# Kernel tuning notes

Hardware: AMD Instinct MI355X
Metric: run time of the kernel (lower is better)

## Reference

```python
import jax, jax.numpy as jnp
import numpy as np

B, S, H = 2, 2048, 1024
NH, KVH, HD = 16, 4, 64
EPS = 1e-6


def setup_inputs() -> dict:
    key = jax.random.key(0)
    ks = jax.random.split(key, 6)
    hidden_states = jax.random.normal(ks[0], (B, S, H), jnp.float32)
    # additive causal mask [B,1,S,S]
    neg = jnp.finfo(jnp.float32).min
    causal = jnp.where(jnp.tril(jnp.ones((S, S), bool)), 0.0, neg)
    attention_mask = jnp.broadcast_to(causal[None, None], (B, 1, S, S))
    # RoPE cos/sin [B,S,HD]
    pos = jnp.arange(S, dtype=jnp.float32)
    inv_freq = 1.0 / (10000.0 ** (jnp.arange(0, HD, 2, dtype=jnp.float32) / HD))
    freqs = pos[:, None] * inv_freq[None, :]          # [S, HD//2]
    emb = jnp.concatenate([freqs, freqs], axis=-1)    # [S, HD]
    cos = jnp.broadcast_to(jnp.cos(emb)[None], (B, S, HD))
    sin = jnp.broadcast_to(jnp.sin(emb)[None], (B, S, HD))
    scale = 0.02
    q_weight = jax.random.normal(ks[1], (NH * HD, H), jnp.float32) * scale
    k_weight = jax.random.normal(ks[2], (KVH * HD, H), jnp.float32) * scale
    v_weight = jax.random.normal(ks[3], (KVH * HD, H), jnp.float32) * scale
    o_weight = jax.random.normal(ks[4], (H, NH * HD), jnp.float32) * scale
    q_norm_weight = jnp.ones((HD,), jnp.float32)
    k_norm_weight = jnp.ones((HD,), jnp.float32)
    return dict(hidden_states=hidden_states, attention_mask=attention_mask,
                cos=cos, sin=sin, q_weight=q_weight, k_weight=k_weight,
                v_weight=v_weight, o_weight=o_weight,
                q_norm_weight=q_norm_weight, k_norm_weight=k_norm_weight)


def _rotate_half(x):
    x1, x2 = x[..., : x.shape[-1] // 2], x[..., x.shape[-1] // 2:]
    return jnp.concatenate([-x2, x1], axis=-1)


def _rms_norm(x, w, eps=EPS):
    xf = x.astype(jnp.float32)
    var = jnp.mean(xf * xf, axis=-1, keepdims=True)
    return (w * (xf * jax.lax.rsqrt(var + eps)).astype(x.dtype))


def reference(hidden_states, attention_mask, cos, sin, q_weight, k_weight,
              v_weight, o_weight, q_norm_weight, k_norm_weight):
    b, s, h = hidden_states.shape
    # projections (torch F.linear: x @ W.T)
    q = (hidden_states @ q_weight.T).reshape(b, s, NH, HD).transpose(0, 2, 1, 3)
    k = (hidden_states @ k_weight.T).reshape(b, s, KVH, HD).transpose(0, 2, 1, 3)
    v = (hidden_states @ v_weight.T).reshape(b, s, KVH, HD).transpose(0, 2, 1, 3)
    # per-head QK RMSNorm (Qwen3 style)
    q = _rms_norm(q, q_norm_weight)
    k = _rms_norm(k, k_norm_weight)
    # RoPE, cos/sin broadcast over head axis
    c, si = cos[:, None], sin[:, None]                 # [B,1,S,HD]
    q = q * c + _rotate_half(q) * si
    k = k * c + _rotate_half(k) * si
    # GQA: repeat kv heads
    rep = NH // KVH
    k = jnp.repeat(k, rep, axis=1)
    v = jnp.repeat(v, rep, axis=1)
    # attention
    scores = jnp.einsum('bhqd,bhkd->bhqk', q, k) * (HD ** -0.5)
    scores = scores + attention_mask[:, :, :, :s]
    attn = jax.nn.softmax(scores.astype(jnp.float32), axis=-1).astype(q.dtype)
    out = jnp.einsum('bhqk,bhkd->bhqd', attn, v)
    out = out.transpose(0, 2, 1, 3).reshape(b, s, NH * HD)
    return out @ o_weight.T
```

## Files before the change

kernel.cpp:

```cpp
#include <hip/hip_runtime.h>

typedef unsigned short u16;
typedef __attribute__((ext_vector_type(4))) float f32x4;
typedef __attribute__((ext_vector_type(8))) __bf16 bf16x8;
typedef __attribute__((ext_vector_type(8))) unsigned short u16x8;
typedef __attribute__((ext_vector_type(4))) unsigned short u16x4;

#define NEGINF -3.0e38f

#define BB 2
#define SS 2048
#define HH 1024
#define NHEAD 16
#define KVHEAD 4
#define HD 64
#define BS (BB*SS)
#define NQKV 1536

#define QSCALE 0.18033688f
#define SMBIAS -11.5415603f

#define PSLOT 8320

__device__ __forceinline__ u16 f2bf(float f) {
  union { float f; unsigned int u; } v; v.f = f;
  unsigned int r = v.u + 0x7FFFu + ((v.u >> 16) & 1u);
  return (u16)(r >> 16);
}
__device__ __forceinline__ float bf2f(u16 h) {
  union { unsigned int u; float f; } v; v.u = ((unsigned int)h) << 16;
  return v.f;
}

typedef const unsigned int __attribute__((address_space(1)))* gp_t;
typedef unsigned int __attribute__((address_space(3)))* lp_t;
__device__ __forceinline__ void gload_lds16(const void* g, void* l) {
  __builtin_amdgcn_global_load_lds((gp_t)g, (lp_t)l, 16, 0, 0);
}

__global__ __launch_bounds__(256) void cvt_all(
    const float* __restrict__ h, const float* __restrict__ qw,
    const float* __restrict__ kw, const float* __restrict__ vw,
    const float* __restrict__ ow,
    u16* __restrict__ Xb, u16* __restrict__ Wqkv, u16* __restrict__ Wo) {
  long i = ((long)blockIdx.x * 256 + threadIdx.x) * 4;
  const float* src; u16* dst;
  if (i < 4194304L)      { src = h  + i;             dst = Xb   + i; }
  else if (i < 5242880L) { src = qw + (i - 4194304); dst = Wqkv + (i - 4194304); }
  else if (i < 5505024L) { src = kw + (i - 5242880); dst = Wqkv + (i - 4194304); }
  else if (i < 5767168L) { src = vw + (i - 5505024); dst = Wqkv + (i - 4194304); }
  else                   { src = ow + (i - 5767168); dst = Wo   + (i - 5767168); }
  float4 v = *(const float4*)src;
  u16x4 o;
  o.x = f2bf(v.x); o.y = f2bf(v.y); o.z = f2bf(v.z); o.w = f2bf(v.w);
  *(u16x4*)dst = o;
}

template<int EPI, int TM>
__global__ __launch_bounds__(256) void gemm_bt(
    const u16* __restrict__ A, const u16* __restrict__ Bw,
    float* __restrict__ Cf,
    u16* __restrict__ Qb, u16* __restrict__ Kb, u16* __restrict__ Vb,
    const float* __restrict__ cosb, const float* __restrict__ sinb,
    const float* __restrict__ qnw, const float* __restrict__ knw,
    int M, int N, int K)
{
  const int AM = TM / 32;
  __shared__ u16 As[2][TM * 64];
  __shared__ u16 Bs[2][128 * 64];
  const int tid = threadIdx.x;
  const int w = tid >> 6, l = tid & 63;
  const int lg = l >> 4, lc = l & 15;
  const int m0 = blockIdx.y * TM, n0 = blockIdx.x * 128;
  const int wr = (w >> 1) * (TM / 2), wc = (w & 1) * 64;

  const f32x4 vzero = {0.f, 0.f, 0.f, 0.f};
  f32x4 acc[AM][4];
#pragma unroll
  for (int i = 0; i < AM; ++i)
#pragma unroll
    for (int j = 0; j < 4; ++j) acc[i][j] = vzero;

  const u16* Ap = A + (size_t)m0 * K;
  const u16* Bp = Bw + (size_t)n0 * K;
  const int nk = K >> 6;

  const int arow = tid >> 3, ach = tid & 7;

#define GSTAGE(bufi, kt)                                                         \
  {                                                                              \
    _Pragma("unroll") for (int c = 0; c < AM; ++c) {                             \
      int row = c * 32 + arow;                                                   \
      gload_lds16(Ap + (size_t)row * K + (kt) * 64 + (ach ^ (row & 7)) * 8,      \
                  (char*)As[bufi] + c * 4096 + w * 1024);                        \
    }                                                                            \
    _Pragma("unroll") for (int c = 0; c < 4; ++c) {                              \
      int row = c * 32 + arow;                                                   \
      gload_lds16(Bp + (size_t)row * K + (kt) * 64 + (ach ^ (row & 7)) * 8,      \
                  (char*)Bs[bufi] + c * 4096 + w * 1024);                        \
    }                                                                            \
  }

  GSTAGE(0, 0)
  __syncthreads();

  for (int kt = 0; kt < nk; ++kt) {
    const int cur = kt & 1;
    if (kt + 1 < nk) GSTAGE(cur ^ 1, kt + 1)

    bf16x8 af[AM][2], bfr[4][2];
#pragma unroll
    for (int i = 0; i < AM; ++i) {
      int row = wr + i * 16 + lc;
#pragma unroll
      for (int c = 0; c < 2; ++c)
        af[i][c] = *(const bf16x8*)&As[cur][row * 64 + (((c * 4 + lg) ^ (lc & 7)) << 3)];
    }
#pragma unroll
    for (int i = 0; i < 4; ++i) {
      int row = wc + i * 16 + lc;
#pragma unroll
      for (int c = 0; c < 2; ++c)
        bfr[i][c] = *(const bf16x8*)&Bs[cur][row * 64 + (((c * 4 + lg) ^ (lc & 7)) << 3)];
    }
    __builtin_amdgcn_s_setprio(1);
#pragma unroll
    for (int c = 0; c < 2; ++c)
#pragma unroll
      for (int am = 0; am < AM; ++am)
#pragma unroll
        for (int bn = 0; bn < 4; ++bn)
          acc[am][bn] = __builtin_amdgcn_mfma_f32_16x16x32_bf16(af[am][c], bfr[bn][c], acc[am][bn], 0, 0, 0);
    __builtin_amdgcn_s_setprio(0);

    if (kt + 1 < nk) __syncthreads();
  }
#undef GSTAGE

  if (EPI == 1) {
#pragma unroll
    for (int am = 0; am < AM; ++am)
#pragma unroll
      for (int bn = 0; bn < 4; ++bn)
#pragma unroll
        for (int r = 0; r < 4; ++r) {
          int m = m0 + wr + am * 16 + lg * 4 + r;
          int n = n0 + wc + bn * 16 + lc;
          Cf[(size_t)m * N + n] = acc[am][bn][r];
        }
  } else {
    const int nb = n0 + wc;
    if (nb < 1280) {
      const bool isQ = (nb < 1024);
      const int head = isQ ? (nb >> 6) : ((nb - 1024) >> 6);
      u16* dst = isQ ? (Qb + ((size_t)head * SS) * HD)
                     : (Kb + ((size_t)head * SS) * HD);
      const size_t hstride = (size_t)(isQ ? NHEAD : KVHEAD) * SS * HD;
      const float* wt = isQ ? qnw : knw;
      const float posc = isQ ? QSCALE : 1.0f;
      float wt4[4];
#pragma unroll
      for (int bn = 0; bn < 4; ++bn) wt4[bn] = wt[bn * 16 + lc];
#pragma unroll
      for (int am = 0; am < AM; ++am)
#pragma unroll
        for (int r = 0; r < 4; ++r) {
          int m = m0 + wr + am * 16 + lg * 4 + r;
          int bb = m >> 11, s2 = m & 2047;
          float ss = 0.f;
#pragma unroll
          for (int bn = 0; bn < 4; ++bn) ss += acc[am][bn][r] * acc[am][bn][r];
          ss += __shfl_xor(ss, 1);
          ss += __shfl_xor(ss, 2);
          ss += __shfl_xor(ss, 4);
          ss += __shfl_xor(ss, 8);
          float rs = rsqrtf(ss * (1.0f / 64.0f) + 1e-6f);
          size_t cbase = ((size_t)bb * SS + s2) * HD;
          size_t obase = bb * hstride + (size_t)s2 * HD;
#pragma unroll
          for (int bn = 0; bn < 4; ++bn) {
            int d = bn * 16 + lc;
            float xn = acc[am][bn][r] * rs * wt4[bn];
            float xp = acc[am][bn ^ 2][r] * rs * wt4[bn ^ 2];
            float rot = (bn < 2) ? -xp : xp;
            float o = (xn * cosb[cbase + d] + rot * sinb[cbase + d]) * posc;
            dst[obase + d] = f2bf(o);
          }
        }
    } else {
      const int kh = (nb - 1280) >> 6;
#pragma unroll
      for (int am = 0; am < AM; ++am)
#pragma unroll
        for (int r = 0; r < 4; ++r) {
          int m = m0 + wr + am * 16 + lg * 4 + r;
          int bb = m >> 11, s2 = m & 2047;
#pragma unroll
          for (int bn = 0; bn < 4; ++bn) {
            int d = bn * 16 + lc;
            Vb[(((size_t)bb * KVHEAD + kh) * HD + d) * SS + s2] = f2bf(acc[am][bn][r]);
          }
        }
    }
  }
}

__global__ __launch_bounds__(256) void attn_kernel(
    const u16* __restrict__ Qb, const u16* __restrict__ Kb,
    const u16* __restrict__ Vt, u16* __restrict__ Ob,
    float* __restrict__ Pw)
{
  __shared__ u16 Ks[2][64 * 64];
  __shared__ u16 Vs[2][64 * 64];

  const int tid = threadIdx.x;
  const int w = tid >> 6, l = tid & 63;
  const int lg = l >> 4, lc = l & 15;

  const int bid = blockIdx.x;
  const int p = bid & 255, half = bid >> 8;
  const int qt_s = p & 7, hb = p >> 3;
  const int h = hb & 15, b = hb >> 4;
  const int qt_l = 15 - qt_s;
  const int L1 = 2 * qt_s + 2;
  const int kvh = h >> 2;

  const u16* Kp = Kb + ((size_t)b * KVHEAD + kvh) * SS * HD;
  const u16* Vp = Vt + ((size_t)b * KVHEAD + kvh) * (size_t)HD * SS;

  const f32x4 vzero = {0.f, 0.f, 0.f, 0.f};
  const f32x4 zbias = {SMBIAS, SMBIAS, SMBIAS, SMBIAS};
  f32x4 acc[2][4];
  float lsum[2] = {0.f, 0.f};
#pragma unroll
  for (int qf = 0; qf < 2; ++qf)
#pragma unroll
    for (int df = 0; df < 4; ++df) acc[qf][df] = vzero;

  const int srow0 = w * 8 + (l >> 3);
  const int srow1 = srow0 + 32;
  const int sswz = (l >> 3) ^ ((w & 1) << 2);
  const int ss0 = (l & 7) ^ sswz;

  int ko[8], vo[8];
#pragma unroll
  for (int f = 0; f < 4; ++f) {
    int row = ((lc >> 2) << 3) + ((f & 1) << 2) + (lc & 3) + ((f >> 1) << 5);
    int swz = (((f & 1) << 2) + (lc & 3)) ^ (((lc >> 2) & 1) << 2);
    ko[2 * f]     = row * 64 + ((lg ^ swz) << 3);
    ko[2 * f + 1] = row * 64 + (((4 + lg) ^ swz) << 3);
  }
#pragma unroll
  for (int df = 0; df < 4; ++df) {
    int vrow = 16 * df + lc;
    int vswz = (lc & 7) ^ (((lc >> 3) & 1) << 2);
    vo[2 * df]     = vrow * 64 + ((lg ^ vswz) << 3);
    vo[2 * df + 1] = vrow * 64 + (((4 + lg) ^ vswz) << 3);
  }

#define STAGE(bufi, kvbase)                                                          \
  gload_lds16(Kp + (size_t)((kvbase) + srow0) * HD + ss0 * 8, (char*)Ks[bufi] + w * 1024);        \
  gload_lds16(Kp + (size_t)((kvbase) + srow1) * HD + ss0 * 8, (char*)Ks[bufi] + 4096 + w * 1024); \
  gload_lds16(Vp + (size_t)srow0 * SS + (kvbase) + ss0 * 8, (char*)Vs[bufi] + w * 1024);          \
  gload_lds16(Vp + (size_t)srow1 * SS + (kvbase) + ss0 * 8, (char*)Vs[bufi] + 4096 + w * 1024);

  auto seg = [&](int qt, int lo, int hi, bool fin) {
    const int q0 = qt * 128;
    const u16* Qp = Qb + (((size_t)b * NHEAD + h) * SS + q0 + w * 32) * HD;
    bf16x8 qa[2][2];
#pragma unroll
    for (int qf = 0; qf < 2; ++qf)
#pragma unroll
      for (int c = 0; c < 2; ++c)
        qa[qf][c] = *(const bf16x8*)(Qp + (qf * 16 + lc) * HD + c * 32 + lg * 8);

    STAGE(0, lo * 64)
    __syncthreads();

    for (int t = lo; t < hi; ++t) {
      const int cur = (t - lo) & 1;
      if (t + 1 < hi) { STAGE(cur ^ 1, (t + 1) * 64) }

      const int kv0 = t * 64;
      if (kv0 <= q0 + w * 32 + 31) {
        const u16* KsB = Ks[cur];
        const u16* VsB = Vs[cur];

        bf16x8 kb[8], vb[8];
#pragma unroll
        for (int i = 0; i < 8; ++i) kb[i] = *(const bf16x8*)&KsB[ko[i]];
#pragma unroll
        for (int i = 0; i < 8; ++i) vb[i] = *(const bf16x8*)&VsB[vo[i]];

        const bool diag = (kv0 + 63 > q0 + w * 32);
        bf16x8 pa[2][2];
#pragma unroll
        for (int c = 0; c < 2; ++c) {
          f32x4 sv[2][2];
#pragma unroll
          for (int fs = 0; fs < 2; ++fs) {
            const int f = 2 * c + fs;
#pragma unroll
            for (int qf = 0; qf < 2; ++qf) {
              f32x4 z = zbias;
              z = __builtin_amdgcn_mfma_f32_16x16x32_bf16(kb[2 * f], qa[qf][0], z, 0, 0, 0);
              z = __builtin_amdgcn_mfma_f32_16x16x32_bf16(kb[2 * f + 1], qa[qf][1], z, 0, 0, 0);
              sv[qf][fs] = z;
            }
          }
          if (diag) {
            const int keyb = kv0 + c * 32 + lg * 8;
#pragma unroll
            for (int qf = 0; qf < 2; ++qf) {
              const int qi = q0 + w * 32 + qf * 16 + lc;
#pragma unroll
              for (int fs = 0; fs < 2; ++fs)
#pragma unroll
                for (int rr = 0; rr < 4; ++rr) {
                  int key = keyb + fs * 4 + rr;
                  if (key > qi) sv[qf][fs][rr] = NEGINF;
                }
            }
          }
#pragma unroll
          for (int qf = 0; qf < 2; ++qf) {
#pragma unroll
            for (int fs = 0; fs < 2; ++fs)
#pragma unroll
              for (int rr = 0; rr < 4; ++rr) {
                float pp = __builtin_amdgcn_exp2f(sv[qf][fs][rr]);
                sv[qf][fs][rr] = pp;
                lsum[qf] += pp;
              }
#pragma unroll
            for (int j = 0; j < 8; ++j)
              pa[qf][c][j] = (__bf16)sv[qf][j >> 2][j & 3];
          }
        }

#pragma unroll
        for (int df = 0; df < 4; ++df)
#pragma unroll
          for (int qf = 0; qf < 2; ++qf) {
            acc[qf][df] = __builtin_amdgcn_mfma_f32_16x16x32_bf16(pa[qf][0], vb[2 * df], acc[qf][df], 0, 0, 0);
            acc[qf][df] = __builtin_amdgcn_mfma_f32_16x16x32_bf16(pa[qf][1], vb[2 * df + 1], acc[qf][df], 0, 0, 0);
          }
      }

      __syncthreads();
    }

    if (fin) {
#pragma unroll
      for (int qf = 0; qf < 2; ++qf) {
        float t = lsum[qf];
        t += __shfl_xor(t, 16);
        t += __shfl_xor(t, 32);
#pragma unroll
        for (int rr = 0; rr < 4; ++rr) {
          float dnm = __shfl(t, lg * 4 + rr);
          float inv = 1.0f / dnm;
          int qi = q0 + w * 32 + qf * 16 + lg * 4 + rr;
#pragma unroll
          for (int df = 0; df < 4; ++df)
            Ob[((size_t)b * SS + qi) * (NHEAD * HD) + h * HD + df * 16 + lc] =
                f2bf(acc[qf][df][rr] * inv);
        }
        lsum[qf] = 0.f;
#pragma unroll
        for (int df = 0; df < 4; ++df) acc[qf][df] = vzero;
      }
    }
  };

  if (half == 0) {
    seg(qt_s, 0, L1, true);
    seg(qt_l, 0, 17 - L1, false);
  } else {
    seg(qt_l, 17 - L1, 2 * qt_l + 2, false);
  }
#undef STAGE

  float* slot = Pw + (size_t)(p * 2 + half) * PSLOT;
#pragma unroll
  for (int qf = 0; qf < 2; ++qf) {
#pragma unroll
    for (int rr = 0; rr < 4; ++rr) {
      int row = w * 32 + qf * 16 + lg * 4 + rr;
#pragma unroll
      for (int df = 0; df < 4; ++df)
        slot[row * 64 + df * 16 + lc] = acc[qf][df][rr];
    }
    float t = lsum[qf];
    t += __shfl_xor(t, 16);
    t += __shfl_xor(t, 32);
    if (l < 16) slot[8192 + w * 32 + qf * 16 + l] = t;
  }
}

__global__ __launch_bounds__(256) void attn_combine(
    const float* __restrict__ Pw, u16* __restrict__ Ob)
{
  const int blk = blockIdx.x;
  const int p = blk >> 1, rh = blk & 1;
  const int qt_s = p & 7, hb = p >> 3;
  const int h = hb & 15, b = hb >> 4;
  const int qt_l = 15 - qt_s;
  const float* A = Pw + (size_t)(p * 2 + 0) * PSLOT;
  const float* Bp = Pw + (size_t)(p * 2 + 1) * PSLOT;
#pragma unroll
  for (int i = 0; i < 16; ++i) {
    int e = i * 256 + threadIdx.x;
    int row = rh * 64 + (e >> 6), d = e & 63;
    float s = A[row * 64 + d] + Bp[row * 64 + d];
    float dn = A[8192 + row] + Bp[8192 + row];
    int qrow = qt_l * 128 + row;
    Ob[((size_t)b * SS + qrow) * (NHEAD * HD) + h * HD + d] = f2bf(s / dn);
  }
}

extern "C" void kernel_launch(void* const* d_in, const int* in_sizes, int n_in,
                              void* d_out, int out_size, void* d_ws, size_t ws_size,
                              hipStream_t stream) {
  const float* hidden = (const float*)d_in[0];
  const float* cosb = (const float*)d_in[2];
  const float* sinb = (const float*)d_in[3];
  const float* qw = (const float*)d_in[4];
  const float* kw = (const float*)d_in[5];
  const float* vw = (const float*)d_in[6];
  const float* ow = (const float*)d_in[7];
  const float* qnw = (const float*)d_in[8];
  const float* knw = (const float*)d_in[9];
  float* out = (float*)d_out;

  u16* Xb   = (u16*)d_ws;
  u16* Wqkv = Xb + (size_t)BS * HH;
  u16* Wo   = Wqkv + (size_t)NQKV * HH;
  u16* Qb   = Wo + (size_t)HH * HH;
  u16* Kb   = Qb + (size_t)BB * NHEAD * SS * HD;
  u16* Vb   = Kb + (size_t)BB * KVHEAD * SS * HD;
  u16* Ab   = Vb + (size_t)BB * KVHEAD * SS * HD;
  float* Pw = (float*)(Ab + (size_t)BS * HH);

  cvt_all<<<6656, 256, 0, stream>>>(hidden, qw, kw, vw, ow, Xb, Wqkv, Wo);

  gemm_bt<0, 128><<<dim3(NQKV / 128, BS / 128), 256, 0, stream>>>(
      Xb, Wqkv, nullptr, Qb, Kb, Vb, cosb, sinb, qnw, knw, BS, NQKV, HH);

  attn_kernel<<<512, 256, 0, stream>>>(Qb, Kb, Vb, Ab, Pw);
  attn_combine<<<512, 256, 0, stream>>>(Pw, Ab);

  gemm_bt<1, 64><<<dim3(HH / 128, BS / 64), 256, 0, stream>>>(
      Ab, Wo, out, nullptr, nullptr, nullptr, nullptr, nullptr, nullptr, nullptr, BS, HH, HH);
}
```

Before: 89.58 us.

## Split causal attention work into three balanced chunks per pair and shrink QKV GEMM tile

Attention work for each (short, long) query-tile pair is now divided across three blocks of about eleven KV tiles each, instead of two uneven halves. Every partial result goes to a workspace slot, and the combine kernel sums one to three slots per query tile. This is meant to balance load and raise occupancy on the many-CU GPU, at the cost of more partial writes and combine reads. Separately, the QKV projection GEMM switches to 64-row M tiles, which doubles its grid size.

```diff
diff --git a/kernel.cpp b/kernel.cpp
--- a/kernel.cpp
+++ b/kernel.cpp
@@ -207,8 +207,7 @@
 
 __global__ __launch_bounds__(256) void attn_kernel(
     const u16* __restrict__ Qb, const u16* __restrict__ Kb,
-    const u16* __restrict__ Vt, u16* __restrict__ Ob,
-    float* __restrict__ Pw)
+    const u16* __restrict__ Vt, float* __restrict__ Pw)
 {
   __shared__ u16 Ks[2][64 * 64];
   __shared__ u16 Vs[2][64 * 64];
@@ -218,7 +217,7 @@
   const int lg = l >> 4, lc = l & 15;
 
   const int bid = blockIdx.x;
-  const int p = bid & 255, half = bid >> 8;
+  const int p = bid & 255, ch = bid >> 8;
   const int qt_s = p & 7, hb = p >> 3;
   const int h = hb & 15, b = hb >> 4;
   const int qt_l = 15 - qt_s;
@@ -264,7 +263,7 @@
   gload_lds16(Vp + (size_t)srow0 * SS + (kvbase) + ss0 * 8, (char*)Vs[bufi] + w * 1024);          \
   gload_lds16(Vp + (size_t)srow1 * SS + (kvbase) + ss0 * 8, (char*)Vs[bufi] + 4096 + w * 1024);
 
-  auto seg = [&](int qt, int lo, int hi, bool fin) {
+  auto seg = [&](int qt, int klo, int khi) {
     const int q0 = qt * 128;
     const u16* Qp = Qb + (((size_t)b * NHEAD + h) * SS + q0 + w * 32) * HD;
     bf16x8 qa[2][2];
@@ -274,12 +273,12 @@
       for (int c = 0; c < 2; ++c)
         qa[qf][c] = *(const bf16x8*)(Qp + (qf * 16 + lc) * HD + c * 32 + lg * 8);
 
-    STAGE(0, lo * 64)
+    STAGE(0, klo * 64)
     __syncthreads();
 
-    for (int t = lo; t < hi; ++t) {
-      const int cur = (t - lo) & 1;
-      if (t + 1 < hi) { STAGE(cur ^ 1, (t + 1) * 64) }
+    for (int t = klo; t < khi; ++t) {
+      const int cur = (t - klo) & 1;
+      if (t + 1 < khi) { STAGE(cur ^ 1, (t + 1) * 64) }
 
       const int kv0 = t * 64;
       if (kv0 <= q0 + w * 32 + 31) {
@@ -349,72 +348,71 @@
 
       __syncthreads();
     }
-
-    if (fin) {
-#pragma unroll
-      for (int qf = 0; qf < 2; ++qf) {
-        float t = lsum[qf];
-        t += __shfl_xor(t, 16);
-        t += __shfl_xor(t, 32);
-#pragma unroll
-        for (int rr = 0; rr < 4; ++rr) {
-          float dnm = __shfl(t, lg * 4 + rr);
-          float inv = 1.0f / dnm;
-          int qi = q0 + w * 32 + qf * 16 + lg * 4 + rr;
-#pragma unroll
-          for (int df = 0; df < 4; ++df)
-            Ob[((size_t)b * SS + qi) * (NHEAD * HD) + h * HD + df * 16 + lc] =
-                f2bf(acc[qf][df][rr] * inv);
-        }
-        lsum[qf] = 0.f;
-#pragma unroll
-        for (int df = 0; df < 4; ++df) acc[qf][df] = vzero;
+  };
+
+  auto wslot = [&](int sidx) {
+    float* slot = Pw + (size_t)(p * 4 + sidx) * PSLOT;
+#pragma unroll
+    for (int qf = 0; qf < 2; ++qf) {
+#pragma unroll
+      for (int rr = 0; rr < 4; ++rr) {
+        int row = w * 32 + qf * 16 + lg * 4 + rr;
+#pragma unroll
+        for (int df = 0; df < 4; ++df)
+          slot[row * 64 + df * 16 + lc] = acc[qf][df][rr];
       }
+      float t = lsum[qf];
+      t += __shfl_xor(t, 16);
+      t += __shfl_xor(t, 32);
+      if (l < 16) slot[8192 + w * 32 + qf * 16 + l] = t;
+      lsum[qf] = 0.f;
+#pragma unroll
+      for (int df = 0; df < 4; ++df) acc[qf][df] = vzero;
     }
   };
 
-  if (half == 0) {
-    seg(qt_s, 0, L1, true);
-    seg(qt_l, 0, 17 - L1, false);
+  if (ch == 0) {
+    seg(qt_s, 0, (L1 < 11) ? L1 : 11);
+    wslot(0);
+    if (L1 < 11) { seg(qt_l, 0, 11 - L1); wslot(1); }
+  } else if (ch == 1) {
+    if (L1 > 11) { seg(qt_s, 11, L1); wslot(1); }
+    seg(qt_l, (L1 < 11) ? (11 - L1) : 0, 22 - L1);
+    wslot(2);
   } else {
-    seg(qt_l, 17 - L1, 2 * qt_l + 2, false);
+    seg(qt_l, 22 - L1, 34 - L1);
+    wslot(3);
   }
 #undef STAGE
-
-  float* slot = Pw + (size_t)(p * 2 + half) * PSLOT;
-#pragma unroll
-  for (int qf = 0; qf < 2; ++qf) {
-#pragma unroll
-    for (int rr = 0; rr < 4; ++rr) {
-      int row = w * 32 + qf * 16 + lg * 4 + rr;
-#pragma unroll
-      for (int df = 0; df < 4; ++df)
-        slot[row * 64 + df * 16 + lc] = acc[qf][df][rr];
-    }
-    float t = lsum[qf];
-    t += __shfl_xor(t, 16);
-    t += __shfl_xor(t, 32);
-    if (l < 16) slot[8192 + w * 32 + qf * 16 + l] = t;
-  }
 }
 
 __global__ __launch_bounds__(256) void attn_combine(
     const float* __restrict__ Pw, u16* __restrict__ Ob)
 {
   const int blk = blockIdx.x;
-  const int p = blk >> 1, rh = blk & 1;
+  const int p = blk >> 1, which = blk & 1;
   const int qt_s = p & 7, hb = p >> 3;
   const int h = hb & 15, b = hb >> 4;
-  const int qt_l = 15 - qt_s;
-  const float* A = Pw + (size_t)(p * 2 + 0) * PSLOT;
-  const float* Bp = Pw + (size_t)(p * 2 + 1) * PSLOT;
-#pragma unroll
-  for (int i = 0; i < 16; ++i) {
+  const int qt = which ? (15 - qt_s) : qt_s;
+  const float* base = Pw + (size_t)p * 4 * PSLOT;
+  const float* S0; const float* S1 = nullptr; const float* S2 = nullptr;
+  if (which == 0) {
+    S0 = base;
+    if (qt_s >= 5) S1 = base + PSLOT;
+  } else {
+    S0 = base + 2 * PSLOT;
+    S1 = base + 3 * PSLOT;
+    if (qt_s <= 4) S2 = base + PSLOT;
+  }
+#pragma unroll
+  for (int i = 0; i < 32; ++i) {
     int e = i * 256 + threadIdx.x;
-    int row = rh * 64 + (e >> 6), d = e & 63;
-    float s = A[row * 64 + d] + Bp[row * 64 + d];
-    float dn = A[8192 + row] + Bp[8192 + row];
-    int qrow = qt_l * 128 + row;
+    int row = e >> 6, d = e & 63;
+    float s = S0[e];
+    float dn = S0[8192 + row];
+    if (S1) { s += S1[e]; dn += S1[8192 + row]; }
+    if (S2) { s += S2[e]; dn += S2[8192 + row]; }
+    int qrow = qt * 128 + row;
     Ob[((size_t)b * SS + qrow) * (NHEAD * HD) + h * HD + d] = f2bf(s / dn);
   }
 }
@@ -444,10 +442,10 @@
 
   cvt_all<<<6656, 256, 0, stream>>>(hidden, qw, kw, vw, ow, Xb, Wqkv, Wo);
 
-  gemm_bt<0, 128><<<dim3(NQKV / 128, BS / 128), 256, 0, stream>>>(
+  gemm_bt<0, 64><<<dim3(NQKV / 128, BS / 64), 256, 0, stream>>>(
       Xb, Wqkv, nullptr, Qb, Kb, Vb, cosb, sinb, qnw, knw, BS, NQKV, HH);
 
-  attn_kernel<<<512, 256, 0, stream>>>(Qb, Kb, Vb, Ab, Pw);
+  attn_kernel<<<768, 256, 0, stream>>>(Qb, Kb, Vb, Pw);
   attn_combine<<<512, 256, 0, stream>>>(Pw, Ab);
 
   gemm_bt<1, 64><<<dim3(HH / 128, BS / 64), 256, 0, stream>>>(
```

Result: slower. 107.0 us (+19.4%).
